# Kernel tuning notes

Hardware: AMD Instinct MI355X
Metric: run time of the kernel (lower is better)

The kernel has to match this reference:

```python
import jax, jax.numpy as jnp
import numpy as np

DIM, HEADS, DHEAD = 256, 8, 64
HID = HEADS * DHEAD


def _elu1(x):
    # F.elu(x) + 1 == exp(x) for x<0, x+1 for x>=0
    return jnp.where(x > 0, x + 1.0, jnp.exp(x))


def setup_inputs() -> dict:
    key = jax.random.key(0)
    ks = jax.random.split(key, 6)
    B, H, W = 8, 64, 64
    x = jax.random.normal(ks[0], (B, DIM, H, W), dtype=jnp.float32)
    contact_map = jax.random.uniform(ks[1], (B, 1, H, W), dtype=jnp.float32)
    s_qkv = 1.0 / np.sqrt(DIM)
    Wqkv = jax.random.normal(ks[2], (3 * HID, DIM), dtype=jnp.float32) * s_qkv
    s_out = 1.0 / np.sqrt(HID)
    Wout = jax.random.normal(ks[3], (DIM, HID), dtype=jnp.float32) * s_out
    bout = jax.random.normal(ks[4], (DIM,), dtype=jnp.float32) * 0.01
    contact_scale = jnp.float32(0.1)
    return {"x": x, "contact_map": contact_map, "Wqkv": Wqkv,
            "Wout": Wout, "bout": bout, "contact_scale": contact_scale}


def reference(x, contact_map, Wqkv, Wout, bout, contact_scale):
    b, c, h, w = x.shape
    n = h * w
    xf = x.reshape(b, c, n)                                  # b c n
    qkv = jnp.einsum('oc,bcn->bon', Wqkv, xf)                # b (3*H*D) n
    qkv = qkv.reshape(b, 3, HEADS, DHEAD, n)                 # qkv-major channel order
    q = _elu1(qkv[:, 0])                                     # b h d n
    k = _elu1(qkv[:, 1])
    v = qkv[:, 2]
    cm = contact_map.reshape(b, 1, 1, n)                     # b 1 1 n
    k = k * (1.0 + contact_scale * cm)
    kv = jnp.einsum('bhdn,bhen->bhde', k, v)                 # b h d e
    ksum = k.sum(axis=-1)                                    # b h d
    z = 1.0 / (jnp.einsum('bhdn,bhd->bhn', q, ksum) + 1e-6)  # b h n
    out = jnp.einsum('bhde,bhdn->bhne', kv, q) * z[..., None]  # b h n e
    out = out.transpose(0, 1, 3, 2).reshape(b, HID, n)       # b (h d) n
    y = jnp.einsum('oc,bcn->bon', Wout, out) + bout[None, :, None]
    return y.reshape(b, -1, h, w)
```

## Files before the change

### kernel.cpp

```cpp
#include <hip/hip_runtime.h>
#include <stdint.h>


#define NPIX 4096
#define HIDC 512
#define DIMC 256
#define BATCH 8

typedef __attribute__((ext_vector_type(8))) short bf16x8;
typedef __attribute__((ext_vector_type(4))) float f32x4;
typedef __attribute__((ext_vector_type(16))) float f32x16;

__device__ __forceinline__ float bf2f(unsigned short h) {
    unsigned int u = ((unsigned int)h) << 16; float f;
    __builtin_memcpy(&f, &u, 4); return f;
}
__device__ __forceinline__ unsigned short f2bf(float f) {
    unsigned int u; __builtin_memcpy(&u, &f, 4);
    u += 0x7fffu + ((u >> 16) & 1u);
    return (unsigned short)(u >> 16);
}
__device__ __forceinline__ float elu1(float x) {
    return x > 0.f ? x + 1.f : __expf(x);
}
__device__ __forceinline__ void gl16(const unsigned short* g, unsigned short* l) {
    __builtin_amdgcn_global_load_lds(
        (__attribute__((address_space(1))) const void*)g,
        (__attribute__((address_space(3))) void*)l, 16, 0, 0);
}

__global__ __launch_bounds__(256) void k_convW(
    const float* __restrict__ Wqkv, const float* __restrict__ Wout,
    unsigned short* __restrict__ Wb, unsigned short* __restrict__ Wob)
{
    int i4 = (blockIdx.x * 256 + threadIdx.x) * 4;
    const int NW1 = 1536 * 256;
    float4 v; unsigned short* dst;
    if (i4 < NW1) { v = *(const float4*)&Wqkv[i4]; dst = Wb + i4; }
    else { int j = i4 - NW1; v = *(const float4*)&Wout[j]; dst = Wob + j; }
    ushort4 o; o.x = f2bf(v.x); o.y = f2bf(v.y); o.z = f2bf(v.z); o.w = f2bf(v.w);
    *(ushort4*)dst = o;
}

__global__ __launch_bounds__(256) void k_tx(
    const float* __restrict__ x, unsigned short* __restrict__ xT)
{
    __shared__ float tile[32][33];
    const int n0 = blockIdx.x * 32, c0 = blockIdx.y * 32, b = blockIdx.z;
    const int t = threadIdx.x;
    const int r = t >> 3, c4 = (t & 7) * 4;
    float4 v = *(const float4*)&x[((size_t)b * DIMC + c0 + r) * NPIX + n0 + c4];
    tile[r][c4 + 0] = v.x; tile[r][c4 + 1] = v.y;
    tile[r][c4 + 2] = v.z; tile[r][c4 + 3] = v.w;
    __syncthreads();
    ushort4 o;
    unsigned short* op = (unsigned short*)&o;
#pragma unroll
    for (int i = 0; i < 4; i++) op[i] = f2bf(tile[c4 + i][r]);
    *(ushort4*)&xT[((size_t)b * NPIX + n0 + r) * DIMC + c0 + c4] = o;
}

__global__ __launch_bounds__(256) void k_qkv(
    const unsigned short* __restrict__ xT,
    const unsigned short* __restrict__ Wb,
    const float* __restrict__ cmp,
    const float* __restrict__ csp,
    unsigned short* __restrict__ qT,
    unsigned short* __restrict__ kb,
    unsigned short* __restrict__ vb)
{
    const int b  = blockIdx.z;
    const int m0 = blockIdx.x * 128;
    const int n0 = blockIdx.y * 128;
    const int t = threadIdx.x;
    const int wave = t >> 6, lane = t & 63;
    const int wm = wave >> 1, wn = wave & 1;
    const int l31 = lane & 31, lhi = lane >> 5;
    const int sect = n0 >> 9;

    __shared__ unsigned short As[128 * 64];
    __shared__ unsigned short Bs[128 * 64];

    const unsigned short* Ag = xT + ((size_t)b * NPIX + m0) * DIMC;
    const unsigned short* Bg = Wb + (size_t)n0 * DIMC;

    const unsigned short* mArr = (sect == 0) ? As : Bs;
    const unsigned short* nArr = (sect == 0) ? Bs : As;

    f32x16 acc[2][2];
#pragma unroll
    for (int i = 0; i < 2; i++)
#pragma unroll
        for (int j = 0; j < 2; j++)
#pragma unroll
            for (int r = 0; r < 16; r++) acc[i][j][r] = 0.f;

    const int r8  = lane >> 3;
    const int jg8 = (((lane & 7) ^ r8) & 7) * 8;
    const int xsw = (l31 & 7);

    for (int k0 = 0; k0 < DIMC; k0 += 64) {
#pragma unroll
        for (int i = 0; i < 4; i++) {
            const int rowg = wave * 32 + i * 8;
            gl16(&Ag[(size_t)(rowg + r8) * DIMC + k0 + jg8], &As[rowg * 64]);
            gl16(&Bg[(size_t)(rowg + r8) * DIMC + k0 + jg8], &Bs[rowg * 64]);
        }
        __syncthreads();
#pragma unroll
        for (int ks = 0; ks < 4; ks++) {
            const int coff = ((ks * 2 + lhi) ^ xsw) * 8;
            bf16x8 af[2], bfg[2];
#pragma unroll
            for (int fm = 0; fm < 2; fm++)
                af[fm] = *(const bf16x8*)&mArr[(wm * 64 + fm * 32 + l31) * 64 + coff];
#pragma unroll
            for (int fn = 0; fn < 2; fn++)
                bfg[fn] = *(const bf16x8*)&nArr[(wn * 64 + fn * 32 + l31) * 64 + coff];
#pragma unroll
            for (int fm = 0; fm < 2; fm++)
#pragma unroll
                for (int fn = 0; fn < 2; fn++)
                    acc[fm][fn] = __builtin_amdgcn_mfma_f32_32x32x16_bf16(
                        af[fm], bfg[fn], acc[fm][fn], 0, 0, 0);
        }
        __syncthreads();
    }

    const float cs = *csp;
    if (sect == 0) {
#pragma unroll
        for (int fm = 0; fm < 2; fm++) {
            const int pbase = m0 + wm * 64 + fm * 32;
#pragma unroll
            for (int fn = 0; fn < 2; fn++) {
                const int o = n0 + wn * 64 + fn * 32 + l31;
#pragma unroll
                for (int r = 0; r < 16; r++) {
                    int prow = pbase + (r & 3) + 8 * (r >> 2) + 4 * lhi;
                    qT[((size_t)b * NPIX + prow) * HIDC + o] = f2bf(elu1(acc[fm][fn][r]));
                }
            }
        }
    } else {
        unsigned short* dstb = (sect == 1) ? kb : vb;
#pragma unroll
        for (int fm = 0; fm < 2; fm++) {
            const int obase = (n0 & 511) + wm * 64 + fm * 32;
#pragma unroll
            for (int fn = 0; fn < 2; fn++) {
                const int pixel = m0 + wn * 64 + fn * 32 + l31;
                float g = 1.f;
                if (sect == 1) g = 1.f + cs * cmp[(size_t)b * NPIX + pixel];
#pragma unroll
                for (int r = 0; r < 16; r++) {
                    int orow = obase + (r & 3) + 8 * (r >> 2) + 4 * lhi;
                    float val = acc[fm][fn][r];
                    if (sect == 1) val = elu1(val) * g;
                    dstb[((size_t)b * HIDC + orow) * NPIX + pixel] = f2bf(val);
                }
            }
        }
    }
}

#define LS2 40
__global__ __launch_bounds__(256) void k_kv(
    const unsigned short* __restrict__ kb, const unsigned short* __restrict__ vb,
    float* __restrict__ kv, float* __restrict__ ksum)
{
    const int bh = blockIdx.y, nc = blockIdx.x;
    const int t = threadIdx.x, wave = t >> 6, lane = t & 63;
    const int lrow = lane & 15, quad = lane >> 4;

    __shared__ unsigned short ks[64 * LS2];
    __shared__ unsigned short vs[64 * LS2];

    const size_t base = (size_t)bh * 64 * NPIX;
    f32x4 acc[4];
#pragma unroll
    for (int i = 0; i < 4; i++) acc[i] = (f32x4){0.f, 0.f, 0.f, 0.f};
    float ksacc = 0.f;

    const int row = t >> 2, c8 = (t & 3) * 8;

    for (int step = 0; step < 16; step++) {
        const int ncol = nc * 512 + step * 32;
        uint4 kq = *(const uint4*)&kb[base + (size_t)row * NPIX + ncol + c8];
        *(uint4*)&ks[row * LS2 + c8] = kq;
        *(uint4*)&vs[row * LS2 + c8] = *(const uint4*)&vb[base + (size_t)row * NPIX + ncol + c8];
        const unsigned short* kp = (const unsigned short*)&kq;
#pragma unroll
        for (int j = 0; j < 8; j++) ksacc += bf2f(kp[j]);
        __syncthreads();
        bf16x8 bfv = *(const bf16x8*)&vs[(wave * 16 + lrow) * LS2 + quad * 8];
#pragma unroll
        for (int mt = 0; mt < 4; mt++) {
            bf16x8 af = *(const bf16x8*)&ks[(mt * 16 + lrow) * LS2 + quad * 8];
            acc[mt] = __builtin_amdgcn_mfma_f32_16x16x32_bf16(af, bfv, acc[mt], 0, 0, 0);
        }
        __syncthreads();
    }

    float* kvb = kv + (size_t)bh * 4096;
#pragma unroll
    for (int mt = 0; mt < 4; mt++)
#pragma unroll
        for (int r = 0; r < 4; r++)
            atomicAdd(&kvb[(mt * 16 + quad * 4 + r) * 64 + wave * 16 + lrow], acc[mt][r]);
    atomicAdd(&ksum[bh * 64 + row], ksacc);
}

#define LS3 72
__global__ __launch_bounds__(256) void k_out(
    const unsigned short* __restrict__ qT,
    const float* __restrict__ kv, const float* __restrict__ ksum,
    unsigned short* __restrict__ outT)
{
    const int bh = blockIdx.y, p0 = blockIdx.x * 128;
    const int b = bh >> 3, h = bh & 7;
    const int t = threadIdx.x, wave = t >> 6, lane = t & 63;
    const int l31 = lane & 31, lhi = lane >> 5;

    __shared__ unsigned short Aq[128 * LS3];
    __shared__ unsigned short Bv[96 * LS3];

    const unsigned short* qg = qT + ((size_t)b * NPIX + p0) * HIDC + h * 64;
#pragma unroll
    for (int i = 0; i < 4; i++) {
        int idx = t + i * 256;
        int row = idx >> 3, c8 = (idx & 7) * 8;
        *(uint4*)&Aq[row * LS3 + c8] = *(const uint4*)&qg[(size_t)row * HIDC + c8];
    }
    const float* kvg = kv + (size_t)bh * 4096;
#pragma unroll
    for (int i = 0; i < 16; i++) {
        int idx = t + i * 256;
        int d = idx >> 6, e = idx & 63;
        Bv[e * LS3 + d] = f2bf(kvg[idx]);
    }
    if (t < 64) {
        float ksv = ksum[bh * 64 + t];
        unsigned short hi = f2bf(ksv);
        Bv[64 * LS3 + t] = hi;
        Bv[65 * LS3 + t] = f2bf(ksv - bf2f(hi));
    }
    for (int i = t; i < 30 * 64; i += 256)
        Bv[(66 + (i >> 6)) * LS3 + (i & 63)] = 0;
    __syncthreads();

    f32x16 acc[3];
#pragma unroll
    for (int j = 0; j < 3; j++)
#pragma unroll
        for (int r = 0; r < 16; r++) acc[j][r] = 0.f;

#pragma unroll
    for (int ksub = 0; ksub < 4; ksub++) {
        const int koff = ksub * 16 + lhi * 8;
        bf16x8 af = *(const bf16x8*)&Aq[(wave * 32 + l31) * LS3 + koff];
#pragma unroll
        for (int nf = 0; nf < 3; nf++) {
            bf16x8 bfg = *(const bf16x8*)&Bv[(nf * 32 + l31) * LS3 + koff];
            acc[nf] = __builtin_amdgcn_mfma_f32_32x32x16_bf16(af, bfg, acc[nf], 0, 0, 0);
        }
    }

    unsigned short* og = outT + ((size_t)b * NPIX + p0 + wave * 32) * HIDC + h * 64;
#pragma unroll
    for (int r = 0; r < 16; r++) {
        float hi = __shfl(acc[2][r], lane & 32);
        float lo = __shfl(acc[2][r], (lane & 32) | 1);
        float z = 1.f / (hi + lo + 1e-6f);
        int prow = (r & 3) + 8 * (r >> 2) + 4 * lhi;
#pragma unroll
        for (int nf = 0; nf < 2; nf++)
            og[(size_t)prow * HIDC + nf * 32 + l31] = f2bf(acc[nf][r] * z);
    }
}

__global__ __launch_bounds__(256) void k_y(
    const unsigned short* __restrict__ outT,
    const unsigned short* __restrict__ Wob,
    const float* __restrict__ bout,
    float* __restrict__ y)
{
    const int b  = blockIdx.z;
    const int m0 = blockIdx.x * 128;
    const int n0 = blockIdx.y * 128;
    const int t = threadIdx.x;
    const int wave = t >> 6, lane = t & 63;
    const int wm = wave >> 1, wn = wave & 1;
    const int lrow = lane & 15, quad = lane >> 4;

    __shared__ unsigned short As[128 * 64];
    __shared__ unsigned short Bs[128 * 64];

    const unsigned short* Ag = outT + ((size_t)b * NPIX + m0) * HIDC;
    const unsigned short* Bg = Wob + (size_t)n0 * HIDC;

    f32x4 acc[4][4];
#pragma unroll
    for (int i = 0; i < 4; i++)
#pragma unroll
        for (int j = 0; j < 4; j++) acc[i][j] = (f32x4){0.f, 0.f, 0.f, 0.f};

    const int r8  = lane >> 3;
    const int jg8 = (((lane & 7) ^ r8) & 7) * 8;
    const int xswA = (lrow & 7);

    for (int k0 = 0; k0 < HIDC; k0 += 64) {
#pragma unroll
        for (int i = 0; i < 4; i++) {
            const int rowg = wave * 32 + i * 8;
            gl16(&Ag[(size_t)(rowg + r8) * HIDC + k0 + jg8], &As[rowg * 64]);
            gl16(&Bg[(size_t)(rowg + r8) * HIDC + k0 + jg8], &Bs[rowg * 64]);
        }
        __syncthreads();
#pragma unroll
        for (int ksb = 0; ksb < 2; ksb++) {
            bf16x8 af[4], bfr[4];
#pragma unroll
            for (int mt = 0; mt < 4; mt++) {
                const int row = wm * 64 + mt * 16 + lrow;
                af[mt] = *(const bf16x8*)&As[row * 64 + (((ksb * 4 + quad) ^ xswA)) * 8];
            }
#pragma unroll
            for (int nt = 0; nt < 4; nt++) {
                const int row = wn * 64 + nt * 16 + lrow;
                bfr[nt] = *(const bf16x8*)&Bs[row * 64 + (((ksb * 4 + quad) ^ xswA)) * 8];
            }
#pragma unroll
            for (int mt = 0; mt < 4; mt++)
#pragma unroll
                for (int nt = 0; nt < 4; nt++)
                    acc[mt][nt] = __builtin_amdgcn_mfma_f32_16x16x32_bf16(
                        af[mt], bfr[nt], acc[mt][nt], 0, 0, 0);
        }
        __syncthreads();
    }

#pragma unroll
    for (int mt = 0; mt < 4; mt++) {
        const int pixel0 = m0 + wm * 64 + mt * 16 + quad * 4;
#pragma unroll
        for (int nt = 0; nt < 4; nt++) {
            const int o = n0 + wn * 64 + nt * 16 + lrow;
            const float bias = bout[o];
            f32x4 a = acc[mt][nt];
            float4 st; st.x = a[0] + bias; st.y = a[1] + bias;
            st.z = a[2] + bias; st.w = a[3] + bias;
            *(float4*)&y[((size_t)b * DIMC + o) * NPIX + pixel0] = st;
        }
    }
}

extern "C" void kernel_launch(void* const* d_in, const int* in_sizes, int n_in,
                              void* d_out, int out_size, void* d_ws, size_t ws_size,
                              hipStream_t stream) {
    (void)in_sizes; (void)n_in; (void)out_size; (void)ws_size;
    const float* x    = (const float*)d_in[0];
    const float* cm   = (const float*)d_in[1];
    const float* Wqkv = (const float*)d_in[2];
    const float* Wout = (const float*)d_in[3];
    const float* bout = (const float*)d_in[4];
    const float* csp  = (const float*)d_in[5];
    float* y = (float*)d_out;

    const size_t qn = (size_t)BATCH * HIDC * NPIX;
    char* ws = (char*)d_ws;
    unsigned short* qT   = (unsigned short*)ws;                 ws += qn * 2;
    unsigned short* kb   = (unsigned short*)ws;                 ws += qn * 2;
    unsigned short* vb   = (unsigned short*)ws;                 ws += qn * 2;
    unsigned short* outT = (unsigned short*)ws;                 ws += qn * 2;
    unsigned short* xT   = outT;
    float* kvp   = (float*)ws;                                  ws += (size_t)64 * 64 * 64 * 4;
    float* ksump = (float*)ws;                                  ws += (size_t)64 * 64 * 4;
    unsigned short* Wb  = (unsigned short*)ws;                  ws += (size_t)1536 * 256 * 2;
    unsigned short* Wob = (unsigned short*)ws;

    hipMemsetAsync(kvp, 0, ((size_t)64 * 64 * 64 + 64 * 64) * sizeof(float), stream);
    k_convW<<<512, 256, 0, stream>>>(Wqkv, Wout, Wb, Wob);
    k_tx  <<<dim3(128, 8, 8), 256, 0, stream>>>(x, xT);
    k_qkv <<<dim3(32, 12, 8), 256, 0, stream>>>(xT, Wb, cm, csp, qT, kb, vb);
    k_kv  <<<dim3(8, 64),     256, 0, stream>>>(kb, vb, kvp, ksump);
    k_out <<<dim3(32, 64),    256, 0, stream>>>(qT, kvp, ksump, outT);
    k_y   <<<dim3(32, 2, 8),  256, 0, stream>>>(outT, Wob, bout, y);
}
```

Measured before the change: 206.3 us.

## Fuse attention-output and output projection kernels, store kv transposed, widen k_kv steps

Merges k_out and k_y into one kernel, k_oy. For each pixel tile and output half it loops over heads, computes the normalized per-head output in LDS and feeds it straight into the Wout projection MFMA, so the bf16 outT intermediate never goes through global memory. k_kv now writes kv transposed so k_oy can load it with vectorized float4 reads, and it processes 64 columns per step, halving its barrier count. The trade-offs are that the per-head q/kv work is recomputed for both output halves, each fused block runs a serial 8-head loop with several barriers, and the grid is smaller (512 blocks).

```diff
diff --git a/kernel.cpp b/kernel.cpp
--- a/kernel.cpp
+++ b/kernel.cpp
@@ -164,17 +164,18 @@
     }
 }
 
-#define LS2 40
+#define LKV 72
 __global__ __launch_bounds__(256) void k_kv(
     const unsigned short* __restrict__ kb, const unsigned short* __restrict__ vb,
-    float* __restrict__ kv, float* __restrict__ ksum)
+    float* __restrict__ kvT,
+    float* __restrict__ ksum)
 {
     const int bh = blockIdx.y, nc = blockIdx.x;
     const int t = threadIdx.x, wave = t >> 6, lane = t & 63;
     const int lrow = lane & 15, quad = lane >> 4;
 
-    __shared__ unsigned short ks[64 * LS2];
-    __shared__ unsigned short vs[64 * LS2];
+    __shared__ unsigned short ks[64 * LKV];
+    __shared__ unsigned short vs[64 * LKV];
 
     const size_t base = (size_t)bh * 64 * NPIX;
     f32x4 acc[4];
@@ -184,173 +185,161 @@
 
     const int row = t >> 2, c8 = (t & 3) * 8;
 
-    for (int step = 0; step < 16; step++) {
-        const int ncol = nc * 512 + step * 32;
-        uint4 kq = *(const uint4*)&kb[base + (size_t)row * NPIX + ncol + c8];
-        *(uint4*)&ks[row * LS2 + c8] = kq;
-        *(uint4*)&vs[row * LS2 + c8] = *(const uint4*)&vb[base + (size_t)row * NPIX + ncol + c8];
-        const unsigned short* kp = (const unsigned short*)&kq;
-#pragma unroll
-        for (int j = 0; j < 8; j++) ksacc += bf2f(kp[j]);
-        __syncthreads();
-        bf16x8 bfv = *(const bf16x8*)&vs[(wave * 16 + lrow) * LS2 + quad * 8];
-#pragma unroll
-        for (int mt = 0; mt < 4; mt++) {
-            bf16x8 af = *(const bf16x8*)&ks[(mt * 16 + lrow) * LS2 + quad * 8];
-            acc[mt] = __builtin_amdgcn_mfma_f32_16x16x32_bf16(af, bfv, acc[mt], 0, 0, 0);
-        }
-        __syncthreads();
-    }
-
-    float* kvb = kv + (size_t)bh * 4096;
+    for (int step = 0; step < 8; step++) {
+        const int ncol = nc * 512 + step * 64;
+        const size_t g = base + (size_t)row * NPIX + ncol;
+        uint4 k0 = *(const uint4*)&kb[g + c8];
+        uint4 k1 = *(const uint4*)&kb[g + c8 + 32];
+        *(uint4*)&ks[row * LKV + c8]      = k0;
+        *(uint4*)&ks[row * LKV + c8 + 32] = k1;
+        *(uint4*)&vs[row * LKV + c8]      = *(const uint4*)&vb[g + c8];
+        *(uint4*)&vs[row * LKV + c8 + 32] = *(const uint4*)&vb[g + c8 + 32];
+        const unsigned short* kp0 = (const unsigned short*)&k0;
+        const unsigned short* kp1 = (const unsigned short*)&k1;
+#pragma unroll
+        for (int j = 0; j < 8; j++) ksacc += bf2f(kp0[j]) + bf2f(kp1[j]);
+        __syncthreads();
+#pragma unroll
+        for (int ks32 = 0; ks32 < 2; ks32++) {
+            bf16x8 bfv = *(const bf16x8*)&vs[(wave * 16 + lrow) * LKV + ks32 * 32 + quad * 8];
+#pragma unroll
+            for (int mt = 0; mt < 4; mt++) {
+                bf16x8 af = *(const bf16x8*)&ks[(mt * 16 + lrow) * LKV + ks32 * 32 + quad * 8];
+                acc[mt] = __builtin_amdgcn_mfma_f32_16x16x32_bf16(af, bfv, acc[mt], 0, 0, 0);
+            }
+        }
+        __syncthreads();
+    }
+
+    float* kvb = kvT + (size_t)bh * 4096;
 #pragma unroll
     for (int mt = 0; mt < 4; mt++)
 #pragma unroll
         for (int r = 0; r < 4; r++)
-            atomicAdd(&kvb[(mt * 16 + quad * 4 + r) * 64 + wave * 16 + lrow], acc[mt][r]);
+            atomicAdd(&kvb[(wave * 16 + lrow) * 64 + mt * 16 + quad * 4 + r], acc[mt][r]);
     atomicAdd(&ksum[bh * 64 + row], ksacc);
 }
 
-#define LS3 72
-__global__ __launch_bounds__(256) void k_out(
+__global__ __launch_bounds__(256) void k_oy(
     const unsigned short* __restrict__ qT,
-    const float* __restrict__ kv, const float* __restrict__ ksum,
-    unsigned short* __restrict__ outT)
-{
-    const int bh = blockIdx.y, p0 = blockIdx.x * 128;
-    const int b = bh >> 3, h = bh & 7;
-    const int t = threadIdx.x, wave = t >> 6, lane = t & 63;
-    const int l31 = lane & 31, lhi = lane >> 5;
-
-    __shared__ unsigned short Aq[128 * LS3];
-    __shared__ unsigned short Bv[96 * LS3];
-
-    const unsigned short* qg = qT + ((size_t)b * NPIX + p0) * HIDC + h * 64;
-#pragma unroll
-    for (int i = 0; i < 4; i++) {
-        int idx = t + i * 256;
-        int row = idx >> 3, c8 = (idx & 7) * 8;
-        *(uint4*)&Aq[row * LS3 + c8] = *(const uint4*)&qg[(size_t)row * HIDC + c8];
-    }
-    const float* kvg = kv + (size_t)bh * 4096;
-#pragma unroll
-    for (int i = 0; i < 16; i++) {
-        int idx = t + i * 256;
-        int d = idx >> 6, e = idx & 63;
-        Bv[e * LS3 + d] = f2bf(kvg[idx]);
-    }
-    if (t < 64) {
-        float ksv = ksum[bh * 64 + t];
-        unsigned short hi = f2bf(ksv);
-        Bv[64 * LS3 + t] = hi;
-        Bv[65 * LS3 + t] = f2bf(ksv - bf2f(hi));
-    }
-    for (int i = t; i < 30 * 64; i += 256)
-        Bv[(66 + (i >> 6)) * LS3 + (i & 63)] = 0;
-    __syncthreads();
-
-    f32x16 acc[3];
-#pragma unroll
-    for (int j = 0; j < 3; j++)
-#pragma unroll
-        for (int r = 0; r < 16; r++) acc[j][r] = 0.f;
-
-#pragma unroll
-    for (int ksub = 0; ksub < 4; ksub++) {
-        const int koff = ksub * 16 + lhi * 8;
-        bf16x8 af = *(const bf16x8*)&Aq[(wave * 32 + l31) * LS3 + koff];
-#pragma unroll
-        for (int nf = 0; nf < 3; nf++) {
-            bf16x8 bfg = *(const bf16x8*)&Bv[(nf * 32 + l31) * LS3 + koff];
-            acc[nf] = __builtin_amdgcn_mfma_f32_32x32x16_bf16(af, bfg, acc[nf], 0, 0, 0);
-        }
-    }
-
-    unsigned short* og = outT + ((size_t)b * NPIX + p0 + wave * 32) * HIDC + h * 64;
-#pragma unroll
-    for (int r = 0; r < 16; r++) {
-        float hi = __shfl(acc[2][r], lane & 32);
-        float lo = __shfl(acc[2][r], (lane & 32) | 1);
-        float z = 1.f / (hi + lo + 1e-6f);
-        int prow = (r & 3) + 8 * (r >> 2) + 4 * lhi;
-#pragma unroll
-        for (int nf = 0; nf < 2; nf++)
-            og[(size_t)prow * HIDC + nf * 32 + l31] = f2bf(acc[nf][r] * z);
-    }
-}
-
-__global__ __launch_bounds__(256) void k_y(
-    const unsigned short* __restrict__ outT,
+    const float* __restrict__ kvT,
+    const float* __restrict__ ksum,
     const unsigned short* __restrict__ Wob,
     const float* __restrict__ bout,
     float* __restrict__ y)
 {
-    const int b  = blockIdx.z;
-    const int m0 = blockIdx.x * 128;
-    const int n0 = blockIdx.y * 128;
-    const int t = threadIdx.x;
-    const int wave = t >> 6, lane = t & 63;
+    const int p0 = blockIdx.x * 128, oh = blockIdx.y, b = blockIdx.z;
+    const int t = threadIdx.x, wave = t >> 6, lane = t & 63;
+    const int l31 = lane & 31, lhi = lane >> 5;
     const int wm = wave >> 1, wn = wave & 1;
-    const int lrow = lane & 15, quad = lane >> 4;
-
-    __shared__ unsigned short As[128 * 64];
-    __shared__ unsigned short Bs[128 * 64];
-
-    const unsigned short* Ag = outT + ((size_t)b * NPIX + m0) * HIDC;
-    const unsigned short* Bg = Wob + (size_t)n0 * HIDC;
-
-    f32x4 acc[4][4];
-#pragma unroll
-    for (int i = 0; i < 4; i++)
-#pragma unroll
-        for (int j = 0; j < 4; j++) acc[i][j] = (f32x4){0.f, 0.f, 0.f, 0.f};
-
-    const int r8  = lane >> 3;
-    const int jg8 = (((lane & 7) ^ r8) & 7) * 8;
-    const int xswA = (lrow & 7);
-
-    for (int k0 = 0; k0 < HIDC; k0 += 64) {
+
+    __shared__ unsigned short Aq[128 * 72];
+    __shared__ unsigned short Bv[96 * 72];
+    __shared__ unsigned short Wo[128 * 64];
+
+    for (int i = t; i < 30 * 64; i += 256)
+        Bv[(66 + (i >> 6)) * 72 + (i & 63)] = 0;
+
+    f32x16 acc2[2][2];
+#pragma unroll
+    for (int i = 0; i < 2; i++)
+#pragma unroll
+        for (int j = 0; j < 2; j++)
+#pragma unroll
+            for (int r = 0; r < 16; r++) acc2[i][j][r] = 0.f;
+
+    for (int h = 0; h < 8; h++) {
+        const int bh = b * 8 + h;
+        const unsigned short* qg = qT + ((size_t)b * NPIX + p0) * HIDC + h * 64;
 #pragma unroll
         for (int i = 0; i < 4; i++) {
-            const int rowg = wave * 32 + i * 8;
-            gl16(&Ag[(size_t)(rowg + r8) * HIDC + k0 + jg8], &As[rowg * 64]);
-            gl16(&Bg[(size_t)(rowg + r8) * HIDC + k0 + jg8], &Bs[rowg * 64]);
-        }
-        __syncthreads();
-#pragma unroll
-        for (int ksb = 0; ksb < 2; ksb++) {
-            bf16x8 af[4], bfr[4];
-#pragma unroll
-            for (int mt = 0; mt < 4; mt++) {
-                const int row = wm * 64 + mt * 16 + lrow;
-                af[mt] = *(const bf16x8*)&As[row * 64 + (((ksb * 4 + quad) ^ xswA)) * 8];
-            }
-#pragma unroll
-            for (int nt = 0; nt < 4; nt++) {
-                const int row = wn * 64 + nt * 16 + lrow;
-                bfr[nt] = *(const bf16x8*)&Bs[row * 64 + (((ksb * 4 + quad) ^ xswA)) * 8];
-            }
-#pragma unroll
-            for (int mt = 0; mt < 4; mt++)
-#pragma unroll
-                for (int nt = 0; nt < 4; nt++)
-                    acc[mt][nt] = __builtin_amdgcn_mfma_f32_16x16x32_bf16(
-                        af[mt], bfr[nt], acc[mt][nt], 0, 0, 0);
-        }
-        __syncthreads();
-    }
-
-#pragma unroll
-    for (int mt = 0; mt < 4; mt++) {
-        const int pixel0 = m0 + wm * 64 + mt * 16 + quad * 4;
-#pragma unroll
-        for (int nt = 0; nt < 4; nt++) {
-            const int o = n0 + wn * 64 + nt * 16 + lrow;
-            const float bias = bout[o];
-            f32x4 a = acc[mt][nt];
-            float4 st; st.x = a[0] + bias; st.y = a[1] + bias;
-            st.z = a[2] + bias; st.w = a[3] + bias;
-            *(float4*)&y[((size_t)b * DIMC + o) * NPIX + pixel0] = st;
+            int idx = t + i * 256;
+            int row = idx >> 3, c8 = (idx & 7) * 8;
+            *(uint4*)&Aq[row * 72 + c8] = *(const uint4*)&qg[(size_t)row * HIDC + c8];
+        }
+        const float* kvg = kvT + (size_t)bh * 4096;
+#pragma unroll
+        for (int i = 0; i < 4; i++) {
+            int idx = t + i * 256;
+            int e = idx >> 4, d4 = (idx & 15) * 4;
+            float4 v = *(const float4*)&kvg[e * 64 + d4];
+            ushort4 o; o.x = f2bf(v.x); o.y = f2bf(v.y); o.z = f2bf(v.z); o.w = f2bf(v.w);
+            *(ushort4*)&Bv[e * 72 + d4] = o;
+        }
+        if (t < 64) {
+            float ksv = ksum[bh * 64 + t];
+            unsigned short hi = f2bf(ksv);
+            Bv[64 * 72 + t] = hi;
+            Bv[65 * 72 + t] = f2bf(ksv - bf2f(hi));
+        }
+#pragma unroll
+        for (int i = 0; i < 4; i++) {
+            int idx = t + i * 256;
+            int o = idx >> 3, c = idx & 7;
+            *(uint4*)&Wo[o * 64 + ((c ^ (o & 7)) * 8)] =
+                *(const uint4*)&Wob[(size_t)(oh * 128 + o) * HIDC + h * 64 + c * 8];
+        }
+        __syncthreads();
+
+        f32x16 a1[3];
+#pragma unroll
+        for (int j = 0; j < 3; j++)
+#pragma unroll
+            for (int r = 0; r < 16; r++) a1[j][r] = 0.f;
+#pragma unroll
+        for (int ksb = 0; ksb < 4; ksb++) {
+            int koff = ksb * 16 + lhi * 8;
+            bf16x8 af = *(const bf16x8*)&Aq[(wave * 32 + l31) * 72 + koff];
+#pragma unroll
+            for (int nf = 0; nf < 3; nf++) {
+                bf16x8 bg = *(const bf16x8*)&Bv[(nf * 32 + l31) * 72 + koff];
+                a1[nf] = __builtin_amdgcn_mfma_f32_32x32x16_bf16(af, bg, a1[nf], 0, 0, 0);
+            }
+        }
+        __syncthreads();
+
+#pragma unroll
+        for (int r = 0; r < 16; r++) {
+            float hi = __shfl(a1[2][r], lane & 32);
+            float lo = __shfl(a1[2][r], (lane & 32) | 1);
+            float z = 1.f / (hi + lo + 1e-6f);
+            int prow = (r & 3) + 8 * (r >> 2) + 4 * lhi;
+#pragma unroll
+            for (int nf = 0; nf < 2; nf++)
+                Aq[(wave * 32 + prow) * 72 + nf * 32 + l31] = f2bf(a1[nf][r] * z);
+        }
+        __syncthreads();
+
+#pragma unroll
+        for (int ksb = 0; ksb < 4; ksb++) {
+            int koff = ksb * 16 + lhi * 8;
+            bf16x8 bg[2];
+#pragma unroll
+            for (int fn = 0; fn < 2; fn++)
+                bg[fn] = *(const bf16x8*)&Aq[(wn * 64 + fn * 32 + l31) * 72 + koff];
+            int wchunk = ((ksb * 2 + lhi) ^ (l31 & 7)) * 8;
+#pragma unroll
+            for (int fm = 0; fm < 2; fm++) {
+                bf16x8 ag = *(const bf16x8*)&Wo[(wm * 64 + fm * 32 + l31) * 64 + wchunk];
+#pragma unroll
+                for (int fn = 0; fn < 2; fn++)
+                    acc2[fm][fn] = __builtin_amdgcn_mfma_f32_32x32x16_bf16(
+                        ag, bg[fn], acc2[fm][fn], 0, 0, 0);
+            }
+        }
+        __syncthreads();
+    }
+
+#pragma unroll
+    for (int fm = 0; fm < 2; fm++) {
+#pragma unroll
+        for (int r = 0; r < 16; r++) {
+            int orow = oh * 128 + wm * 64 + fm * 32 + (r & 3) + 8 * (r >> 2) + 4 * lhi;
+            float bias = bout[orow];
+#pragma unroll
+            for (int fn = 0; fn < 2; fn++)
+                y[((size_t)b * DIMC + orow) * NPIX + p0 + wn * 64 + fn * 32 + l31] =
+                    acc2[fm][fn][r] + bias;
         }
     }
 }
@@ -369,11 +358,10 @@
 
     const size_t qn = (size_t)BATCH * HIDC * NPIX;
     char* ws = (char*)d_ws;
-    unsigned short* qT   = (unsigned short*)ws;                 ws += qn * 2;
-    unsigned short* kb   = (unsigned short*)ws;                 ws += qn * 2;
-    unsigned short* vb   = (unsigned short*)ws;                 ws += qn * 2;
-    unsigned short* outT = (unsigned short*)ws;                 ws += qn * 2;
-    unsigned short* xT   = outT;
+    unsigned short* qT  = (unsigned short*)ws;                  ws += qn * 2;
+    unsigned short* kb  = (unsigned short*)ws;                  ws += qn * 2;
+    unsigned short* vb  = (unsigned short*)ws;                  ws += qn * 2;
+    unsigned short* xT  = (unsigned short*)ws;                  ws += qn * 2;
     float* kvp   = (float*)ws;                                  ws += (size_t)64 * 64 * 64 * 4;
     float* ksump = (float*)ws;                                  ws += (size_t)64 * 64 * 4;
     unsigned short* Wb  = (unsigned short*)ws;                  ws += (size_t)1536 * 256 * 2;
@@ -384,6 +372,5 @@
     k_tx  <<<dim3(128, 8, 8), 256, 0, stream>>>(x, xT);
     k_qkv <<<dim3(32, 12, 8), 256, 0, stream>>>(xT, Wb, cm, csp, qT, kb, vb);
     k_kv  <<<dim3(8, 64),     256, 0, stream>>>(kb, vb, kvp, ksump);
-    k_out <<<dim3(32, 64),    256, 0, stream>>>(qT, kvp, ksump, outT);
-    k_y   <<<dim3(32, 2, 8),  256, 0, stream>>>(outT, Wob, bout, y);
-}
+    k_oy  <<<dim3(32, 2, 8),  256, 0, stream>>>(qT, kvp, ksump, Wob, bout, y);
+}
```

After: 234.0 us. 13.4% more time.
